# Optimization experiments

Hardware: AMD Instinct MI355X
Metric: run time of the kernel (lower is better)

Reference implementation:

```python
import jax, jax.numpy as jnp
import numpy as np

K = 3      # deformable kernel size
PAD = 1    # padding for all 3x3 convs


def conv2d(x, w, b):
    y = jax.lax.conv_general_dilated(x, w, (1, 1), ((PAD, PAD), (PAD, PAD)),
                                     dimension_numbers=('NCHW', 'OIHW', 'NCHW'))
    return y + b[None, :, None, None]


def ln_channels(x, w, b, eps=1e-5):
    # Restormer 'WithBias' LayerNorm: normalize over channel dim of NCHW
    mu = jnp.mean(x, axis=1, keepdims=True)
    var = jnp.mean((x - mu) ** 2, axis=1, keepdims=True)
    return (x - mu) / jnp.sqrt(var + eps) * w[None, :, None, None] + b[None, :, None, None]


def deform_conv(x, offset, mask, weight, bias):
    # x: [B,Cin,H,W], offset: [B,2*K*K,H,W] (dy,dx interleaved), mask: [B,K*K,H,W]
    B, Cin, H, W = x.shape
    Kk = K * K
    off = offset.reshape(B, Kk, 2, H, W)
    dy, dx = off[:, :, 0], off[:, :, 1]                     # [B,Kk,H,W]
    ky, kx = jnp.meshgrid(jnp.arange(K), jnp.arange(K), indexing='ij')
    ky = (ky.reshape(-1) - PAD).astype(x.dtype)             # [Kk]
    kx = (kx.reshape(-1) - PAD).astype(x.dtype)
    py = jnp.arange(H, dtype=x.dtype)[None, None, :, None] + ky[None, :, None, None] + dy
    px = jnp.arange(W, dtype=x.dtype)[None, None, None, :] + kx[None, :, None, None] + dx
    y0 = jnp.floor(py); x0 = jnp.floor(px)
    wy1 = py - y0; wx1 = px - x0
    xf = x.reshape(B, Cin, H * W)

    def corner(yc, xc, wgt):
        valid = (yc >= 0) & (yc <= H - 1) & (xc >= 0) & (xc <= W - 1)
        yi = jnp.clip(yc, 0, H - 1).astype(jnp.int32)
        xi = jnp.clip(xc, 0, W - 1).astype(jnp.int32)
        idx = (yi * W + xi).reshape(B, -1)                  # [B, Kk*H*W]
        v = jax.vmap(lambda xb, ib: xb[:, ib])(xf, idx)     # [B, Cin, Kk*H*W]
        v = v.reshape(B, Cin, Kk, H, W)
        return v * (wgt * valid.astype(x.dtype))[:, None]

    sampled = (corner(y0, x0, (1 - wy1) * (1 - wx1))
               + corner(y0, x0 + 1, (1 - wy1) * wx1)
               + corner(y0 + 1, x0, wy1 * (1 - wx1))
               + corner(y0 + 1, x0 + 1, wy1 * wx1))         # [B,Cin,Kk,H,W]
    sampled = sampled * mask[:, None]                        # modulated (DCNv2)
    wk = weight.reshape(weight.shape[0], Cin, Kk)            # [Cout,Cin,Kk]
    out = jnp.einsum('bckhw,ock->bohw', sampled, wk)
    return out + bias[None, :, None, None]


def setup_inputs() -> dict:
    key = jax.random.key(0)
    ks = jax.random.split(key, 12)
    B, Ce, Cf, H, W = 4, 32, 64, 128, 128
    Cin, Kk = Ce + Cf, K * K
    d = {
        'f_evt_rec': jax.random.normal(ks[0], (B, Ce, H, W), jnp.float32),
        'f_efnet':   jax.random.normal(ks[1], (B, Cf, H, W), jnp.float32),
        'ln_evt_w': jnp.ones((Ce,), jnp.float32), 'ln_evt_b': jnp.zeros((Ce,), jnp.float32),
        'ln_ef_w':  jnp.ones((Cf,), jnp.float32), 'ln_ef_b':  jnp.zeros((Cf,), jnp.float32),
        'ln_al_w':  jnp.ones((Cf,), jnp.float32), 'ln_al_b':  jnp.zeros((Cf,), jnp.float32),
        'off_w': jax.random.normal(ks[2], (2 * Kk, Cin, K, K), jnp.float32) * 0.01,
        'off_b': jnp.zeros((2 * Kk,), jnp.float32),
        'mod_w': jax.random.normal(ks[3], (Kk, Cin, K, K), jnp.float32) * 0.01,
        'mod_b': jnp.zeros((Kk,), jnp.float32),
        'reg_w': jax.random.normal(ks[4], (Cf, Cin, K, K), jnp.float32) * 0.05,
        'reg_b': jnp.zeros((Cf,), jnp.float32),
        'stage_idx': 0,
    }
    return d


def reference(f_evt_rec, f_efnet, ln_evt_w, ln_evt_b, ln_ef_w, ln_ef_b,
              ln_al_w, ln_al_b, off_w, off_b, mod_w, mod_b, reg_w, reg_b, stage_idx):
    e = ln_channels(f_evt_rec, ln_evt_w, ln_evt_b)
    fe = ln_channels(f_efnet, ln_ef_w, ln_ef_b)
    ox = jnp.concatenate([e, fe], axis=1)                    # [B,96,H,W]
    offset = conv2d(ox, off_w, off_b)
    mask = 2.0 * jax.nn.sigmoid(conv2d(ox, mod_w, mod_b))
    al = deform_conv(ox, offset, mask, reg_w, reg_b)         # [B,64,H,W]
    al = jnp.where(al >= 0, al, 0.2 * al)                    # LeakyReLU(0.2)
    al = ln_channels(al, ln_al_w, ln_al_b)
    return al
```

## Files before the change

### kernel.cpp

```cpp
#include <hip/hip_runtime.h>
#include <hip/hip_bf16.h>

#define BATCH 4
#define HH 128
#define WW 128
#define CE 32
#define CF 64
#define CIN 96
#define KK 9
#define COUT 64

typedef __bf16 bf16x8 __attribute__((ext_vector_type(8)));
typedef float f32x4 __attribute__((ext_vector_type(4)));

#define MFMA16(a, b, c) __builtin_amdgcn_mfma_f32_16x16x32_bf16(a, b, c, 0, 0, 0)

#define OX_BYTES   (BATCH * HH * WW * CIN * 2)
#define OFFM_OFFB  OX_BYTES
#define OFFM_BYTES (BATCH * HH * WW * 27 * 4)
#define WCT_OFFB   (OFFM_OFFB + OFFM_BYTES)
#define WCT_BYTES  (32 * 864 * 2)
#define WKT_OFFB   (WCT_OFFB + WCT_BYTES)
#define WKT_BYTES  (64 * 864 * 2)

__global__ void prep_weights(const float* __restrict__ off_w,
                             const float* __restrict__ mod_w,
                             const float* __restrict__ reg_w,
                             __hip_bfloat16* __restrict__ wcombT,
                             __hip_bfloat16* __restrict__ wkT) {
  int e = blockIdx.x * 256 + threadIdx.x;
  const int TOT1 = 32 * 864;
  const int TOT2 = 64 * 864;
  if (e < TOT1) {
    int oc = e / 864, k = e % 864;
    int tap = k / 96, c = k % 96;
    float v = 0.f;
    if (oc < 18)      v = off_w[(oc * CIN + c) * KK + tap];
    else if (oc < 27) v = mod_w[((oc - 18) * CIN + c) * KK + tap];
    wcombT[e] = __float2bfloat16(v);
  } else if (e < TOT1 + TOT2) {
    int e2 = e - TOT1;
    int oc = e2 / 864, k = e2 % 864;
    int tap = k / 96, c = k % 96;
    wkT[e2] = __float2bfloat16(reg_w[(oc * CIN + c) * KK + tap]);
  }
}

__global__ __launch_bounds__(128) void ln_concat(
    const float* __restrict__ evt, const float* __restrict__ efn,
    const float* __restrict__ w_e, const float* __restrict__ b_e,
    const float* __restrict__ w_f, const float* __restrict__ b_f,
    __hip_bfloat16* __restrict__ ox) {
  __shared__ float vals[WW * 97];
  __shared__ float mu_e[WW], rs_e[WW], mu_f[WW], rs_f[WW];
  __shared__ float lnw[CIN], lnb[CIN];
  int t = threadIdx.x;
  int b = blockIdx.x >> 7, y = blockIdx.x & 127;
  if (t < CIN) {
    lnw[t] = (t < CE) ? w_e[t] : w_f[t - CE];
    lnb[t] = (t < CE) ? b_e[t] : b_f[t - CE];
  }
  int x = t;
  float s = 0.f, s2 = 0.f;
  const float* pe = evt + ((size_t)(b * CE) * HH + y) * WW + x;
  for (int c = 0; c < CE; ++c) {
    float v = pe[(size_t)c * HH * WW];
    vals[x * 97 + c] = v;
    s += v; s2 += v * v;
  }
  float mu = s * (1.f / CE);
  float var = s2 * (1.f / CE) - mu * mu;
  mu_e[x] = mu; rs_e[x] = rsqrtf(var + 1e-5f);
  s = 0.f; s2 = 0.f;
  const float* pf = efn + ((size_t)(b * CF) * HH + y) * WW + x;
  for (int c = 0; c < CF; ++c) {
    float v = pf[(size_t)c * HH * WW];
    vals[x * 97 + CE + c] = v;
    s += v; s2 += v * v;
  }
  mu = s * (1.f / CF);
  var = s2 * (1.f / CF) - mu * mu;
  mu_f[x] = mu; rs_f[x] = rsqrtf(var + 1e-5f);
  __syncthreads();
  uint* orow = (uint*)(ox + (size_t)blockIdx.x * WW * CIN);
  for (int i = 0; i < 48; ++i) {
    int g = i * 128 + t;
    int xx = g / 48, c = (g % 48) * 2;
    float v0 = vals[xx * 97 + c], v1 = vals[xx * 97 + c + 1];
    float o0 = (c < CE) ? (v0 - mu_e[xx]) * rs_e[xx] : (v0 - mu_f[xx]) * rs_f[xx];
    float o1 = (c + 1 < CE) ? (v1 - mu_e[xx]) * rs_e[xx] : (v1 - mu_f[xx]) * rs_f[xx];
    o0 = o0 * lnw[c] + lnb[c];
    o1 = o1 * lnw[c + 1] + lnb[c + 1];
    __hip_bfloat16 h0 = __float2bfloat16(o0), h1 = __float2bfloat16(o1);
    orow[g] = ((uint)*(unsigned short*)&h1 << 16) | (uint)*(unsigned short*)&h0;
  }
}

__global__ __launch_bounds__(256) void conv_offmask_mfma(
    const __hip_bfloat16* __restrict__ ox,
    const __hip_bfloat16* __restrict__ wcombT,
    const float* __restrict__ off_b, const float* __restrict__ mod_b,
    float* __restrict__ offm) {
  __shared__ char smem[47872];
  short* At = (short*)smem;
  short* Bt = (short*)(smem + 41184);
  float* outl = (float*)smem;

  int t = threadIdx.x;
  int p0 = blockIdx.x * 64;
  int b = p0 >> 14;
  int y = (p0 >> 7) & 127;
  int x0 = p0 & 127;

  for (int u = t; u < 3 * 66 * 12; u += 256) {
    int c8 = u % 12;
    int pw = u / 12;
    int w = pw % 66;
    int r = pw / 66;
    int yy = y + r - 1;
    int xx = x0 + w - 1;
    uint4 v = {0u, 0u, 0u, 0u};
    if ((unsigned)yy < 128u && (unsigned)xx < 128u)
      v = *(const uint4*)(ox + (size_t)((b << 14) + (yy << 7) + xx) * CIN + c8 * 8);
    *(uint4*)&At[(r * 66 + w) * 104 + c8 * 8] = v;
  }

  int lane = t & 63;
  int wv = t >> 6;
  int mw = wv >> 1, nw = wv & 1;
  int lr = lane & 15, lg = lane >> 4;

  f32x4 acc0 = {0.f, 0.f, 0.f, 0.f}, acc1 = {0.f, 0.f, 0.f, 0.f};

  for (int tap = 0; tap < 9; ++tap) {
    for (int u = t; u < 384; u += 256) {
      int c8 = u % 12, oc = u / 12;
      *(uint4*)&Bt[oc * 104 + c8 * 8] =
          *(const uint4*)(wcombT + oc * 864 + tap * 96 + c8 * 8);
    }
    __syncthreads();
    int dy = tap / 3, dx = tap % 3;
#pragma unroll
    for (int ks = 0; ks < 3; ++ks) {
      int ko = ks * 32 + lg * 8;
      bf16x8 bf = *(const bf16x8*)&Bt[(nw * 16 + lr) * 104 + ko];
      bf16x8 a0 = *(const bf16x8*)&At[(dy * 66 + mw * 32 + lr + dx) * 104 + ko];
      bf16x8 a1 = *(const bf16x8*)&At[(dy * 66 + mw * 32 + 16 + lr + dx) * 104 + ko];
      acc0 = MFMA16(a0, bf, acc0);
      acc1 = MFMA16(a1, bf, acc1);
    }
    __syncthreads();
  }

  int oc = nw * 16 + lr;
  float bia = 0.f;
  if (oc < 18) bia = off_b[oc];
  else if (oc < 27) bia = mod_b[oc - 18];
#pragma unroll
  for (int mi = 0; mi < 2; ++mi) {
    f32x4 a = mi ? acc1 : acc0;
#pragma unroll
    for (int r = 0; r < 4; ++r) {
      int px = mw * 32 + mi * 16 + lg * 4 + r;
      if (oc < 27) {
        float v = a[r] + bia;
        if (oc >= 18) v = 2.f / (1.f + __expf(-v));
        outl[px * 28 + oc] = v;
      }
    }
  }
  __syncthreads();
  for (int e = t; e < 64 * 27; e += 256) {
    int px = e / 27, c = e % 27;
    offm[(size_t)p0 * 27 + e] = outl[px * 28 + c];
  }
}

__global__ __launch_bounds__(256) void deform_ln_mfma(
    const __hip_bfloat16* __restrict__ ox,
    const float* __restrict__ offm,
    const __hip_bfloat16* __restrict__ wkT,
    const float* __restrict__ reg_b,
    const float* __restrict__ lnw, const float* __restrict__ lnb,
    float* __restrict__ out) {
  __shared__ char smem[28672];
  int*   sI = (int*)smem;
  float* sW = (float*)(smem + 1024);
  short* Sa = (short*)(smem + 2048);
  short* Wk = (short*)(smem + 15360);
  float* outl = (float*)(smem + 2048);

  int t = threadIdx.x;
  int p0 = blockIdx.x * 64;
  int b = p0 >> 14;
  int y = (p0 >> 7) & 127;
  int x0 = p0 & 127;
  const __hip_bfloat16* oxb = ox + ((size_t)b << 14) * CIN;

  int lane = t & 63, wv = t >> 6;
  int mw = wv >> 1, nw = wv & 1;
  int lr = lane & 15, lg = lane >> 4;

  f32x4 a00 = {0.f,0.f,0.f,0.f}, a01 = {0.f,0.f,0.f,0.f};
  f32x4 a10 = {0.f,0.f,0.f,0.f}, a11 = {0.f,0.f,0.f,0.f};

  for (int tap = 0; tap < 9; ++tap) {
    for (int u = t; u < 768; u += 256) {
      int c8 = u % 12, oc = u / 12;
      *(uint4*)&Wk[oc * 104 + c8 * 8] =
          *(const uint4*)(wkT + oc * 864 + tap * 96 + c8 * 8);
    }
    if (t < 64) {
      int px = t;
      const float* om = offm + (size_t)(p0 + px) * 27;
      float dyv = om[2 * tap], dxv = om[2 * tap + 1], mk = om[18 + tap];
      float psy = (float)(y + tap / 3 - 1) + dyv;
      float psx = (float)(x0 + px + tap % 3 - 1) + dxv;
      float fy = floorf(psy), fx = floorf(psx);
      float wy1 = psy - fy, wx1 = psx - fx;
      float wy0 = 1.f - wy1, wx0 = 1.f - wx1;
      int iy0 = (int)fy, ix0 = (int)fx;
      int iy1 = iy0 + 1, ix1 = ix0 + 1;
      float vy0 = ((unsigned)iy0 < 128u) ? 1.f : 0.f;
      float vy1 = ((unsigned)iy1 < 128u) ? 1.f : 0.f;
      float vx0 = ((unsigned)ix0 < 128u) ? 1.f : 0.f;
      float vx1 = ((unsigned)ix1 < 128u) ? 1.f : 0.f;
      int cy0 = min(max(iy0, 0), 127), cy1 = min(max(iy1, 0), 127);
      int cx0 = min(max(ix0, 0), 127), cx1 = min(max(ix1, 0), 127);
      sI[px * 4 + 0] = ((cy0 << 7) + cx0) * CIN;
      sI[px * 4 + 1] = ((cy0 << 7) + cx1) * CIN;
      sI[px * 4 + 2] = ((cy1 << 7) + cx0) * CIN;
      sI[px * 4 + 3] = ((cy1 << 7) + cx1) * CIN;
      sW[px * 4 + 0] = wy0 * wx0 * vy0 * vx0 * mk;
      sW[px * 4 + 1] = wy0 * wx1 * vy0 * vx1 * mk;
      sW[px * 4 + 2] = wy1 * wx0 * vy1 * vx0 * mk;
      sW[px * 4 + 3] = wy1 * wx1 * vy1 * vx1 * mk;
    }
    __syncthreads();
#pragma unroll
    for (int it = 0; it < 3; ++it) {
      int u = it * 256 + t;
      int px = u / 12, c8 = u % 12;
      const int* si = sI + px * 4;
      const float* sw = sW + px * 4;
      uint4 q0 = *(const uint4*)(oxb + si[0] + c8 * 8);
      uint4 q1 = *(const uint4*)(oxb + si[1] + c8 * 8);
      uint4 q2 = *(const uint4*)(oxb + si[2] + c8 * 8);
      uint4 q3 = *(const uint4*)(oxb + si[3] + c8 * 8);
      float w0 = sw[0], w1 = sw[1], w2 = sw[2], w3 = sw[3];
      uint rr[4];
#pragma unroll
      for (int j = 0; j < 4; ++j) {
        uint u0 = ((uint*)&q0)[j], u1 = ((uint*)&q1)[j];
        uint u2 = ((uint*)&q2)[j], u3 = ((uint*)&q3)[j];
        float lo = w0 * __uint_as_float(u0 << 16) + w1 * __uint_as_float(u1 << 16)
                 + w2 * __uint_as_float(u2 << 16) + w3 * __uint_as_float(u3 << 16);
        float hi = w0 * __uint_as_float(u0 & 0xffff0000u) + w1 * __uint_as_float(u1 & 0xffff0000u)
                 + w2 * __uint_as_float(u2 & 0xffff0000u) + w3 * __uint_as_float(u3 & 0xffff0000u);
        __hip_bfloat16 bl = __float2bfloat16(lo);
        __hip_bfloat16 bh = __float2bfloat16(hi);
        rr[j] = ((uint)*(unsigned short*)&bh << 16) | (uint)*(unsigned short*)&bl;
      }
      uint4 rv = {rr[0], rr[1], rr[2], rr[3]};
      *(uint4*)&Sa[px * 104 + c8 * 8] = rv;
    }
    __syncthreads();
#pragma unroll
    for (int ks = 0; ks < 3; ++ks) {
      int ko = ks * 32 + lg * 8;
      bf16x8 fa0 = *(const bf16x8*)&Sa[(mw * 32 + lr) * 104 + ko];
      bf16x8 fa1 = *(const bf16x8*)&Sa[(mw * 32 + 16 + lr) * 104 + ko];
      bf16x8 fb0 = *(const bf16x8*)&Wk[(nw * 32 + lr) * 104 + ko];
      bf16x8 fb1 = *(const bf16x8*)&Wk[(nw * 32 + 16 + lr) * 104 + ko];
      a00 = MFMA16(fa0, fb0, a00);
      a01 = MFMA16(fa0, fb1, a01);
      a10 = MFMA16(fa1, fb0, a10);
      a11 = MFMA16(fa1, fb1, a11);
    }
    __syncthreads();
  }

#pragma unroll
  for (int mi = 0; mi < 2; ++mi)
#pragma unroll
  for (int ni = 0; ni < 2; ++ni) {
    int oc = nw * 32 + ni * 16 + lr;
    float bia = reg_b[oc];
    f32x4 a = (mi == 0) ? (ni == 0 ? a00 : a01) : (ni == 0 ? a10 : a11);
#pragma unroll
    for (int r = 0; r < 4; ++r) {
      int px = mw * 32 + mi * 16 + lg * 4 + r;
      float v = a[r] + bia;
      v = (v >= 0.f) ? v : 0.2f * v;
      outl[px * 68 + oc] = v;
    }
  }
  __syncthreads();

  {
    int px = t >> 2, part = t & 3;
    float s = 0.f, s2 = 0.f;
#pragma unroll
    for (int j = 0; j < 16; ++j) {
      float v = outl[px * 68 + part * 16 + j];
      s += v; s2 += v * v;
    }
    s += __shfl_xor(s, 1); s2 += __shfl_xor(s2, 1);
    s += __shfl_xor(s, 2); s2 += __shfl_xor(s2, 2);
    float mu = s * (1.f / 64.f);
    float var = s2 * (1.f / 64.f) - mu * mu;
    float rs = rsqrtf(var + 1e-5f);
    size_t ob = (size_t)b * COUT * 16384 + (size_t)y * 128 + x0 + px;
#pragma unroll
    for (int j = 0; j < 16; ++j) {
      int oc = part * 16 + j;
      float v = outl[px * 68 + oc];
      out[ob + (size_t)oc * 16384] = (v - mu) * rs * lnw[oc] + lnb[oc];
    }
  }
}

extern "C" void kernel_launch(void* const* d_in, const int* in_sizes, int n_in,
                              void* d_out, int out_size, void* d_ws, size_t ws_size,
                              hipStream_t stream) {
  const float* evt      = (const float*)d_in[0];
  const float* efn      = (const float*)d_in[1];
  const float* ln_evt_w = (const float*)d_in[2];
  const float* ln_evt_b = (const float*)d_in[3];
  const float* ln_ef_w  = (const float*)d_in[4];
  const float* ln_ef_b  = (const float*)d_in[5];
  const float* ln_al_w  = (const float*)d_in[6];
  const float* ln_al_b  = (const float*)d_in[7];
  const float* off_w    = (const float*)d_in[8];
  const float* off_b    = (const float*)d_in[9];
  const float* mod_w    = (const float*)d_in[10];
  const float* mod_b    = (const float*)d_in[11];
  const float* reg_w    = (const float*)d_in[12];
  const float* reg_b    = (const float*)d_in[13];
  float* out = (float*)d_out;

  char* wsb = (char*)d_ws;
  __hip_bfloat16* oxb    = (__hip_bfloat16*)wsb;
  float*          offm   = (float*)(wsb + OFFM_OFFB);
  __hip_bfloat16* wcombT = (__hip_bfloat16*)(wsb + WCT_OFFB);
  __hip_bfloat16* wkT    = (__hip_bfloat16*)(wsb + WKT_OFFB);

  prep_weights<<<(32 * 864 + 64 * 864 + 255) / 256, 256, 0, stream>>>(
      off_w, mod_w, reg_w, wcombT, wkT);
  ln_concat<<<BATCH * HH, 128, 0, stream>>>(
      evt, efn, ln_evt_w, ln_evt_b, ln_ef_w, ln_ef_b, oxb);
  conv_offmask_mfma<<<BATCH * HH * WW / 64, 256, 0, stream>>>(
      oxb, wcombT, off_b, mod_b, offm);
  deform_ln_mfma<<<BATCH * HH * WW / 64, 256, 0, stream>>>(
      oxb, offm, wkT, reg_b, ln_al_w, ln_al_b, out);
}
```

Measured before the change: 181.1 us.

## Load conv operands directly from global, double-buffer deform samples, swizzle block order

The offset/mask conv drops its LDS staging of the input halo and weights. Each lane now loads its MFMA A and B fragments straight from global memory with bounds masking, which removes all the per-tap barriers. The deform kernel precomputes bilinear indices and weights for all 9 taps up front, reads weight fragments directly from global, and ping-pongs the sampled tile between two LDS buffers so each tap needs one barrier instead of two. Both kernels also remap block IDs to interleave rows for L2 locality, at the cost of more global/L2 traffic per MFMA and larger LDS use in the deform kernel.

```diff
diff --git a/kernel.cpp b/kernel.cpp
--- a/kernel.cpp
+++ b/kernel.cpp
@@ -14,6 +14,8 @@
 typedef float f32x4 __attribute__((ext_vector_type(4)));
 
 #define MFMA16(a, b, c) __builtin_amdgcn_mfma_f32_16x16x32_bf16(a, b, c, 0, 0, 0)
+
+typedef union { uint4 u; bf16x8 v; } U8;
 
 #define OX_BYTES   (BATCH * HH * WW * CIN * 2)
 #define OFFM_OFFB  OX_BYTES
@@ -101,55 +103,48 @@
     const __hip_bfloat16* __restrict__ wcombT,
     const float* __restrict__ off_b, const float* __restrict__ mod_b,
     float* __restrict__ offm) {
-  __shared__ char smem[47872];
-  short* At = (short*)smem;
-  short* Bt = (short*)(smem + 41184);
-  float* outl = (float*)smem;
-
-  int t = threadIdx.x;
-  int p0 = blockIdx.x * 64;
+  __shared__ float outl[64 * 28];
+
+  int bid = blockIdx.x;
+  int wg = (bid & 7) * 128 + (bid >> 3);
+  int p0 = wg * 64;
   int b = p0 >> 14;
   int y = (p0 >> 7) & 127;
   int x0 = p0 & 127;
 
-  for (int u = t; u < 3 * 66 * 12; u += 256) {
-    int c8 = u % 12;
-    int pw = u / 12;
-    int w = pw % 66;
-    int r = pw / 66;
-    int yy = y + r - 1;
-    int xx = x0 + w - 1;
-    uint4 v = {0u, 0u, 0u, 0u};
-    if ((unsigned)yy < 128u && (unsigned)xx < 128u)
-      v = *(const uint4*)(ox + (size_t)((b << 14) + (yy << 7) + xx) * CIN + c8 * 8);
-    *(uint4*)&At[(r * 66 + w) * 104 + c8 * 8] = v;
-  }
-
-  int lane = t & 63;
-  int wv = t >> 6;
+  int t = threadIdx.x, lane = t & 63, wv = t >> 6;
   int mw = wv >> 1, nw = wv & 1;
   int lr = lane & 15, lg = lane >> 4;
 
+  const __hip_bfloat16* oxb = ox + (((size_t)b) << 14) * CIN;
+  const __hip_bfloat16* brow = wcombT + (size_t)(nw * 16 + lr) * 864;
+
   f32x4 acc0 = {0.f, 0.f, 0.f, 0.f}, acc1 = {0.f, 0.f, 0.f, 0.f};
 
+#pragma unroll
   for (int tap = 0; tap < 9; ++tap) {
-    for (int u = t; u < 384; u += 256) {
-      int c8 = u % 12, oc = u / 12;
-      *(uint4*)&Bt[oc * 104 + c8 * 8] =
-          *(const uint4*)(wcombT + oc * 864 + tap * 96 + c8 * 8);
-    }
-    __syncthreads();
-    int dy = tap / 3, dx = tap % 3;
+    int dy = tap / 3 - 1, dx = tap % 3 - 1;
+    int yy = y + dy;
+    int xx0 = x0 + mw * 32 + lr + dx;
+    int xx1 = xx0 + 16;
+    bool v0 = ((unsigned)yy < 128u) && ((unsigned)xx0 < 128u);
+    bool v1 = ((unsigned)yy < 128u) && ((unsigned)xx1 < 128u);
+    int cy = min(max(yy, 0), 127);
+    int cx0 = min(max(xx0, 0), 127);
+    int cx1 = min(max(xx1, 0), 127);
+    const __hip_bfloat16* arow = oxb + ((size_t)(cy << 7)) * CIN;
 #pragma unroll
     for (int ks = 0; ks < 3; ++ks) {
       int ko = ks * 32 + lg * 8;
-      bf16x8 bf = *(const bf16x8*)&Bt[(nw * 16 + lr) * 104 + ko];
-      bf16x8 a0 = *(const bf16x8*)&At[(dy * 66 + mw * 32 + lr + dx) * 104 + ko];
-      bf16x8 a1 = *(const bf16x8*)&At[(dy * 66 + mw * 32 + 16 + lr + dx) * 104 + ko];
-      acc0 = MFMA16(a0, bf, acc0);
-      acc1 = MFMA16(a1, bf, acc1);
-    }
-    __syncthreads();
+      U8 a0, a1, bf;
+      a0.u = *(const uint4*)(arow + cx0 * CIN + ko);
+      a1.u = *(const uint4*)(arow + cx1 * CIN + ko);
+      if (!v0) { a0.u.x = 0; a0.u.y = 0; a0.u.z = 0; a0.u.w = 0; }
+      if (!v1) { a1.u.x = 0; a1.u.y = 0; a1.u.z = 0; a1.u.w = 0; }
+      bf.u = *(const uint4*)(brow + tap * 96 + ko);
+      acc0 = MFMA16(a0.v, bf.v, acc0);
+      acc1 = MFMA16(a1.v, bf.v, acc1);
+    }
   }
 
   int oc = nw * 16 + lr;
@@ -183,66 +178,69 @@
     const float* __restrict__ reg_b,
     const float* __restrict__ lnw, const float* __restrict__ lnb,
     float* __restrict__ out) {
-  __shared__ char smem[28672];
-  int*   sI = (int*)smem;
-  float* sW = (float*)(smem + 1024);
-  short* Sa = (short*)(smem + 2048);
-  short* Wk = (short*)(smem + 15360);
-  float* outl = (float*)(smem + 2048);
-
-  int t = threadIdx.x;
-  int p0 = blockIdx.x * 64;
+  __shared__ char smem[45056];
+  int*   sI  = (int*)smem;
+  float* sW  = (float*)(smem + 9216);
+  short* SaA = (short*)(smem + 18432);
+  short* SaB = (short*)(smem + 31744);
+  float* outl = (float*)smem;
+
+  int bid = blockIdx.x;
+  int wg = (bid & 7) * 128 + (bid >> 3);
+  int p0 = wg * 64;
   int b = p0 >> 14;
   int y = (p0 >> 7) & 127;
   int x0 = p0 & 127;
-  const __hip_bfloat16* oxb = ox + ((size_t)b << 14) * CIN;
-
-  int lane = t & 63, wv = t >> 6;
+  const __hip_bfloat16* oxb = ox + (((size_t)b) << 14) * CIN;
+
+  int t = threadIdx.x, lane = t & 63, wv = t >> 6;
   int mw = wv >> 1, nw = wv & 1;
   int lr = lane & 15, lg = lane >> 4;
 
+  for (int u = t; u < 576; u += 256) {
+    int px = u & 63, tap = u >> 6;
+    const float* om = offm + (size_t)(p0 + px) * 27;
+    float dyv = om[2 * tap], dxv = om[2 * tap + 1], mk = om[18 + tap];
+    float psy = (float)(y + tap / 3 - 1) + dyv;
+    float psx = (float)(x0 + px + tap % 3 - 1) + dxv;
+    float fy = floorf(psy), fx = floorf(psx);
+    float wy1 = psy - fy, wx1 = psx - fx;
+    float wy0 = 1.f - wy1, wx0 = 1.f - wx1;
+    int iy0 = (int)fy, ix0 = (int)fx;
+    int iy1 = iy0 + 1, ix1 = ix0 + 1;
+    float vy0 = ((unsigned)iy0 < 128u) ? 1.f : 0.f;
+    float vy1 = ((unsigned)iy1 < 128u) ? 1.f : 0.f;
+    float vx0 = ((unsigned)ix0 < 128u) ? 1.f : 0.f;
+    float vx1 = ((unsigned)ix1 < 128u) ? 1.f : 0.f;
+    int cy0 = min(max(iy0, 0), 127), cy1 = min(max(iy1, 0), 127);
+    int cx0 = min(max(ix0, 0), 127), cx1 = min(max(ix1, 0), 127);
+    int base = u * 4;
+    sI[base + 0] = ((cy0 << 7) + cx0) * CIN;
+    sI[base + 1] = ((cy0 << 7) + cx1) * CIN;
+    sI[base + 2] = ((cy1 << 7) + cx0) * CIN;
+    sI[base + 3] = ((cy1 << 7) + cx1) * CIN;
+    sW[base + 0] = wy0 * wx0 * vy0 * vx0 * mk;
+    sW[base + 1] = wy0 * wx1 * vy0 * vx1 * mk;
+    sW[base + 2] = wy1 * wx0 * vy1 * vx0 * mk;
+    sW[base + 3] = wy1 * wx1 * vy1 * vx1 * mk;
+  }
+  __syncthreads();
+
   f32x4 a00 = {0.f,0.f,0.f,0.f}, a01 = {0.f,0.f,0.f,0.f};
   f32x4 a10 = {0.f,0.f,0.f,0.f}, a11 = {0.f,0.f,0.f,0.f};
 
+  const __hip_bfloat16* wb0 = wkT + (size_t)(nw * 32 + lr) * 864;
+  const __hip_bfloat16* wb1 = wkT + (size_t)(nw * 32 + 16 + lr) * 864;
+
   for (int tap = 0; tap < 9; ++tap) {
-    for (int u = t; u < 768; u += 256) {
-      int c8 = u % 12, oc = u / 12;
-      *(uint4*)&Wk[oc * 104 + c8 * 8] =
-          *(const uint4*)(wkT + oc * 864 + tap * 96 + c8 * 8);
-    }
-    if (t < 64) {
-      int px = t;
-      const float* om = offm + (size_t)(p0 + px) * 27;
-      float dyv = om[2 * tap], dxv = om[2 * tap + 1], mk = om[18 + tap];
-      float psy = (float)(y + tap / 3 - 1) + dyv;
-      float psx = (float)(x0 + px + tap % 3 - 1) + dxv;
-      float fy = floorf(psy), fx = floorf(psx);
-      float wy1 = psy - fy, wx1 = psx - fx;
-      float wy0 = 1.f - wy1, wx0 = 1.f - wx1;
-      int iy0 = (int)fy, ix0 = (int)fx;
-      int iy1 = iy0 + 1, ix1 = ix0 + 1;
-      float vy0 = ((unsigned)iy0 < 128u) ? 1.f : 0.f;
-      float vy1 = ((unsigned)iy1 < 128u) ? 1.f : 0.f;
-      float vx0 = ((unsigned)ix0 < 128u) ? 1.f : 0.f;
-      float vx1 = ((unsigned)ix1 < 128u) ? 1.f : 0.f;
-      int cy0 = min(max(iy0, 0), 127), cy1 = min(max(iy1, 0), 127);
-      int cx0 = min(max(ix0, 0), 127), cx1 = min(max(ix1, 0), 127);
-      sI[px * 4 + 0] = ((cy0 << 7) + cx0) * CIN;
-      sI[px * 4 + 1] = ((cy0 << 7) + cx1) * CIN;
-      sI[px * 4 + 2] = ((cy1 << 7) + cx0) * CIN;
-      sI[px * 4 + 3] = ((cy1 << 7) + cx1) * CIN;
-      sW[px * 4 + 0] = wy0 * wx0 * vy0 * vx0 * mk;
-      sW[px * 4 + 1] = wy0 * wx1 * vy0 * vx1 * mk;
-      sW[px * 4 + 2] = wy1 * wx0 * vy1 * vx0 * mk;
-      sW[px * 4 + 3] = wy1 * wx1 * vy1 * vx1 * mk;
-    }
-    __syncthreads();
+    short* S = (tap & 1) ? SaB : SaA;
 #pragma unroll
     for (int it = 0; it < 3; ++it) {
       int u = it * 256 + t;
       int px = u / 12, c8 = u % 12;
-      const int* si = sI + px * 4;
-      const float* sw = sW + px * 4;
+      int pb = (tap * 64 + px) * 4;
+      const int* si = sI + pb;
+      const float* sw = sW + pb;
       uint4 q0 = *(const uint4*)(oxb + si[0] + c8 * 8);
       uint4 q1 = *(const uint4*)(oxb + si[1] + c8 * 8);
       uint4 q2 = *(const uint4*)(oxb + si[2] + c8 * 8);
@@ -262,23 +260,24 @@
         rr[j] = ((uint)*(unsigned short*)&bh << 16) | (uint)*(unsigned short*)&bl;
       }
       uint4 rv = {rr[0], rr[1], rr[2], rr[3]};
-      *(uint4*)&Sa[px * 104 + c8 * 8] = rv;
+      *(uint4*)&S[px * 104 + c8 * 8] = rv;
     }
     __syncthreads();
 #pragma unroll
     for (int ks = 0; ks < 3; ++ks) {
       int ko = ks * 32 + lg * 8;
-      bf16x8 fa0 = *(const bf16x8*)&Sa[(mw * 32 + lr) * 104 + ko];
-      bf16x8 fa1 = *(const bf16x8*)&Sa[(mw * 32 + 16 + lr) * 104 + ko];
-      bf16x8 fb0 = *(const bf16x8*)&Wk[(nw * 32 + lr) * 104 + ko];
-      bf16x8 fb1 = *(const bf16x8*)&Wk[(nw * 32 + 16 + lr) * 104 + ko];
-      a00 = MFMA16(fa0, fb0, a00);
-      a01 = MFMA16(fa0, fb1, a01);
-      a10 = MFMA16(fa1, fb0, a10);
-      a11 = MFMA16(fa1, fb1, a11);
-    }
-    __syncthreads();
-  }
+      bf16x8 fa0 = *(const bf16x8*)&S[(mw * 32 + lr) * 104 + ko];
+      bf16x8 fa1 = *(const bf16x8*)&S[(mw * 32 + 16 + lr) * 104 + ko];
+      U8 b0, b1;
+      b0.u = *(const uint4*)(wb0 + tap * 96 + ko);
+      b1.u = *(const uint4*)(wb1 + tap * 96 + ko);
+      a00 = MFMA16(fa0, b0.v, a00);
+      a01 = MFMA16(fa0, b1.v, a01);
+      a10 = MFMA16(fa1, b0.v, a10);
+      a11 = MFMA16(fa1, b1.v, a11);
+    }
+  }
+  __syncthreads();
 
 #pragma unroll
   for (int mi = 0; mi < 2; ++mi)
```

Result: faster. 176.0 us (-2.8%).
